# Kernel optimization log

Measured on AMD Instinct MI355X. Metric: run time of the kernel, lower is better.

## Reference

```python
import jax, jax.numpy as jnp
import numpy as np

B = 64
RX, RZ, RX_, RZ_ = 32, 16, 16, 8
TN = 1
STRIDE = 2
IN_DIM, OUT_DIM = 256, 512
KEY_DIM, H, ATTN_RATIO = 32, 8, 2
D = ATTN_RATIO * KEY_DIM            # per-head value dim = 64
DH = D * H                          # 512
NH_KD = KEY_DIM * H                 # 256
N = RX * RX + TN * RZ * RZ          # 1280 tokens (search + template)
N_ = RX_ * RX_ + TN * RZ_ * RZ_     # 320 subsampled query tokens
SCALE = KEY_DIM ** -0.5
EPS = 1e-5


def linear_bn(x, W, gamma, beta):
    # Linear (no bias) followed by BatchNorm1d in training mode over (B*N, C)
    y = jnp.einsum('bnc,oc->bno', x, W)
    m = y.mean(axis=(0, 1))
    v = y.var(axis=(0, 1))  # biased variance, as torch BN uses for normalization
    return (y - m) * jax.lax.rsqrt(v + EPS) * gamma + beta


def subsample(x):
    # stride-subsample the search-region tokens and each template's tokens
    b, n, c = x.shape
    parts = [x[:, :RX * RX].reshape(b, RX, RX, c)[:, ::STRIDE, ::STRIDE].reshape(b, -1, c)]
    for i in range(TN):
        s = RX * RX + i * RZ * RZ
        z = x[:, s:s + RZ * RZ].reshape(b, RZ, RZ, c)[:, ::STRIDE, ::STRIDE].reshape(b, -1, c)
        parts.append(z)
    return jnp.concatenate(parts, axis=1)


def setup_inputs() -> dict:
    key = jax.random.key(0)
    ks = jax.random.split(key, 4)
    return {
        'x': jax.random.normal(ks[0], (B, N, IN_DIM), dtype=jnp.float32),
        'W_kv': jax.random.normal(ks[1], (NH_KD + DH, IN_DIM), dtype=jnp.float32) * 0.02,
        'g_kv': jnp.ones((NH_KD + DH,), jnp.float32),
        'b_kv': jnp.zeros((NH_KD + DH,), jnp.float32),
        'W_q': jax.random.normal(ks[2], (NH_KD, IN_DIM), dtype=jnp.float32) * 0.02,
        'g_q': jnp.ones((NH_KD,), jnp.float32),
        'b_q': jnp.zeros((NH_KD,), jnp.float32),
        'W_p': jax.random.normal(ks[3], (OUT_DIM, DH), dtype=jnp.float32) * 0.02,
        'g_p': jnp.ones((OUT_DIM,), jnp.float32),
        'b_p': jnp.zeros((OUT_DIM,), jnp.float32),
    }


def reference(x, W_kv, g_kv, b_kv, W_q, g_q, b_q, W_p, g_p, b_p):
    b = x.shape[0]
    # fused KV projection + BN, then split into per-head K and V
    kv = linear_bn(x, W_kv, g_kv, b_kv).reshape(b, N, H, KEY_DIM + D)
    k = kv[..., :KEY_DIM].transpose(0, 2, 1, 3)   # [B,H,N,key_dim]
    v = kv[..., KEY_DIM:].transpose(0, 2, 1, 3)   # [B,H,N,d]
    # Q: subsample tokens, then Linear_BN
    q = linear_bn(subsample(x), W_q, g_q, b_q).reshape(b, N_, H, KEY_DIM).transpose(0, 2, 1, 3)
    attn = jax.nn.softmax(jnp.einsum('bhqd,bhkd->bhqk', q, k) * SCALE, axis=-1)
    o = jnp.einsum('bhqk,bhkd->bhqd', attn, v).transpose(0, 2, 1, 3).reshape(b, N_, DH)
    return linear_bn(jax.nn.hard_swish(o), W_p, g_p, b_p)
```

## Files before the change

### kernel.cpp

```cpp
#include <hip/hip_runtime.h>
#include <hip/hip_bf16.h>
#include <math.h>

#define EPSF 1e-5f
#define SCALEF 0.17677669529663687f
#define LOG2E 1.4426950408889634f

typedef unsigned short u16;
typedef unsigned int u32;
typedef __attribute__((ext_vector_type(8))) short bf16x8;
typedef __attribute__((ext_vector_type(4))) float f32x4;

__device__ __forceinline__ float b2f(u16 u) {
    union { unsigned int i; float f; } v; v.i = ((unsigned int)u) << 16; return v.f;
}
__device__ __forceinline__ u16 f2b(float f) {
    union { float f; unsigned int i; } v; v.f = f;
    unsigned int x = v.i;
    return (u16)((x + 0x7fffu + ((x >> 16) & 1u)) >> 16);
}
__device__ __forceinline__ float fexp2(float x) {
#if __has_builtin(__builtin_amdgcn_exp2f)
    return __builtin_amdgcn_exp2f(x);
#else
    return exp2f(x);
#endif
}
__device__ __forceinline__ u32 cvtpk_bf16(float lo, float hi) {
    u32 r;
    asm("v_cvt_pk_bf16_f32 %0, %1, %2" : "=v"(r) : "v"(lo), "v"(hi));
    return r;
}
__device__ __forceinline__ void gload_lds16(const u16* __restrict__ g, u16* l) {
    __builtin_amdgcn_global_load_lds(
        (const __attribute__((address_space(1))) void*)g,
        (__attribute__((address_space(3))) void*)l, 16, 0, 0);
}

__global__ void convert_f32_bf16(const float* __restrict__ src, u16* __restrict__ dst, int n4) {
    int i = blockIdx.x * 256 + threadIdx.x;
    if (i >= n4) return;
    float4 v = ((const float4*)src)[i];
    ushort4 o;
    o.x = f2b(v.x); o.y = f2b(v.y); o.z = f2b(v.z); o.w = f2b(v.w);
    ((ushort4*)dst)[i] = o;
}

__global__ void convert_wkv_perm(const float* __restrict__ W, u16* __restrict__ out) {
    int r = blockIdx.x, cl = threadIdx.x;
    int src = (r < 256) ? ((r >> 5) * 96 + (r & 31))
                        : (((r - 256) >> 6) * 96 + 32 + ((r - 256) & 63));
    out[r * 256 + cl] = f2b(W[src * 256 + cl]);
}

__global__ void gather_sub_bf16(const u16* __restrict__ xb, u16* __restrict__ xsub, int n8) {
    int i = blockIdx.x * 256 + threadIdx.x;
    if (i >= n8) return;
    int e = i << 3;
    int row = e >> 8;
    int col = e & 255;
    int b = row / 320;
    int t = row - b * 320;
    int n;
    if (t < 256) n = ((t >> 4) << 6) + ((t & 15) << 1);
    else { int tt = t - 256; n = 1024 + ((tt >> 3) << 5) + ((tt & 7) << 1); }
    *(int4*)(xsub + e) = *(const int4*)(xb + ((size_t)(b * 1280 + n)) * 256 + col);
}

template<int MODE>
__global__ __launch_bounds__(256) void gemm_bt(const u16* __restrict__ A, const u16* __restrict__ Bw,
                                               void* __restrict__ Cv, void* __restrict__ C2v,
                                               int M, int N, int K,
                                               float* __restrict__ sums) {
    __shared__ u16 As[2][128 * 32];
    __shared__ u16 Bs[2][128 * 32];
    __shared__ float sumbuf[4][64][2];
    const int tid = threadIdx.x;
    const int wave = tid >> 6, lane = tid & 63;
    const int quad = lane >> 4, lc = lane & 15;
    const int wr = wave >> 1, wc = wave & 1;
    const int m0 = blockIdx.y * 128, n0 = blockIdx.x * 128;

    const int srow = (wave << 5) + (lane >> 2);
    const int scol = (lane & 3) << 3;
    const int ldsoff = (wave << 5) * 32;
    const u16* gA0 = A  + (size_t)(m0 + srow) * K + scol;
    const u16* gA1 = A  + (size_t)(m0 + srow + 16) * K + scol;
    const u16* gB0 = Bw + (size_t)(n0 + srow) * K + scol;
    const u16* gB1 = Bw + (size_t)(n0 + srow + 16) * K + scol;

    f32x4 acc[4][4];
#pragma unroll
    for (int i = 0; i < 4; ++i)
#pragma unroll
        for (int j = 0; j < 4; ++j) acc[i][j] = (f32x4){0.f, 0.f, 0.f, 0.f};

    auto STAGE = [&](int buf, int k0) {
        gload_lds16(gA0 + k0, &As[buf][ldsoff]);
        gload_lds16(gA1 + k0, &As[buf][ldsoff + 16 * 32]);
        gload_lds16(gB0 + k0, &Bs[buf][ldsoff]);
        gload_lds16(gB1 + k0, &Bs[buf][ldsoff + 16 * 32]);
    };

    STAGE(0, 0);
    int cur = 0;
    for (int k0 = 0; k0 < K; k0 += 32) {
        if (k0 + 32 < K) {
            STAGE(cur ^ 1, k0 + 32);
            asm volatile("s_waitcnt vmcnt(4)" ::: "memory");
        } else {
            asm volatile("s_waitcnt vmcnt(0)" ::: "memory");
        }
        __builtin_amdgcn_s_barrier();
        bf16x8 af[4], bfr[4];
#pragma unroll
        for (int mi = 0; mi < 4; ++mi) af[mi]  = *(const bf16x8*)&As[cur][(wr * 64 + mi * 16 + lc) * 32 + quad * 8];
#pragma unroll
        for (int ni = 0; ni < 4; ++ni) bfr[ni] = *(const bf16x8*)&Bs[cur][(wc * 64 + ni * 16 + lc) * 32 + quad * 8];
#pragma unroll
        for (int mi = 0; mi < 4; ++mi)
#pragma unroll
            for (int ni = 0; ni < 4; ++ni)
                acc[mi][ni] = __builtin_amdgcn_mfma_f32_16x16x32_bf16(af[mi], bfr[ni], acc[mi][ni], 0, 0, 0);
        __builtin_amdgcn_s_barrier();
        cur ^= 1;
    }

    float ps[4], ps2[4];
#pragma unroll
    for (int ni = 0; ni < 4; ++ni) { ps[ni] = 0.f; ps2[ni] = 0.f; }
#pragma unroll
    for (int mi = 0; mi < 4; ++mi)
#pragma unroll
        for (int ni = 0; ni < 4; ++ni)
#pragma unroll
            for (int r = 0; r < 4; ++r) {
                float v = acc[mi][ni][r];
                ps[ni] += v; ps2[ni] += v * v;
            }

    if (MODE == 0 || MODE == 1) {
#pragma unroll
        for (int mi = 0; mi < 4; ++mi)
#pragma unroll
            for (int ni = 0; ni < 4; ++ni)
#pragma unroll
                for (int r = 0; r < 4; ++r) {
                    int row = m0 + wr * 64 + mi * 16 + quad * 4 + r;
                    int cn  = n0 + wc * 64 + ni * 16 + lc;
                    float v = acc[mi][ni][r];
                    if (MODE == 1) ((float*)Cv)[(size_t)row * N + cn] = v;
                    else           ((u16*)Cv)[(size_t)row * N + cn] = f2b(v);
                }
    } else if (n0 < 256) {
        u16* Kr = (u16*)Cv;
#pragma unroll
        for (int mi = 0; mi < 4; ++mi)
#pragma unroll
            for (int r = 0; r < 4; ++r) {
                int t = m0 + wr * 64 + mi * 16 + quad * 4 + r;
                int kk = t & 31;
                int pr = (t & ~31) + ((kk & 4) << 2) + ((kk >> 3) << 2) + (kk & 3);
#pragma unroll
                for (int ni = 0; ni < 4; ++ni) {
                    int c = n0 + wc * 64 + ni * 16 + lc;
                    Kr[(size_t)pr * 256 + c] = f2b(acc[mi][ni][r]);
                }
            }
    } else {
        u16* Vt = (u16*)C2v;
#pragma unroll
        for (int mi = 0; mi < 4; ++mi)
#pragma unroll
            for (int ni = 0; ni < 4; ++ni) {
                int cp = n0 - 256 + wc * 64 + ni * 16 + lc;
                int t0 = m0 + wr * 64 + mi * 16 + quad * 4;
                uint2 w;
                w.x = cvtpk_bf16(acc[mi][ni][0], acc[mi][ni][1]);
                w.y = cvtpk_bf16(acc[mi][ni][2], acc[mi][ni][3]);
                *(uint2*)(Vt + (size_t)cp * 81920 + t0) = w;
            }
    }

#pragma unroll
    for (int ni = 0; ni < 4; ++ni) {
        ps[ni]  += __shfl_xor(ps[ni], 16);  ps[ni]  += __shfl_xor(ps[ni], 32);
        ps2[ni] += __shfl_xor(ps2[ni], 16); ps2[ni] += __shfl_xor(ps2[ni], 32);
    }
    if (quad == 0) {
#pragma unroll
        for (int ni = 0; ni < 4; ++ni) {
            sumbuf[wave][ni * 16 + lc][0] = ps[ni];
            sumbuf[wave][ni * 16 + lc][1] = ps2[ni];
        }
    }
    __syncthreads();
    {
        int which = tid & 1, idx = (tid >> 1) & 63, wcg = tid >> 7;
        int channel = n0 + wcg * 64 + idx;
        float v = sumbuf[wcg][idx][which] + sumbuf[wcg + 2][idx][which];
        int rep = blockIdx.y & 7;
        atomicAdd(&sums[(rep * 2 + which) * N + channel], v);
    }
}

__global__ void finalize_bn(const float* __restrict__ sum2, const float* __restrict__ g,
                            const float* __restrict__ beta, int cols, float inv_n, float scale,
                            float* __restrict__ AB, int kvperm) {
    int c = blockIdx.x * 256 + threadIdx.x;
    if (c >= cols) return;
    float s = 0.f, s2 = 0.f;
#pragma unroll
    for (int r = 0; r < 8; ++r) {
        s  += sum2[(r * 2 + 0) * cols + c];
        s2 += sum2[(r * 2 + 1) * cols + c];
    }
    int src = c;
    if (kvperm) {
        src = (c < 256) ? ((c >> 5) * 96 + (c & 31))
                        : (((c - 256) >> 6) * 96 + 32 + ((c - 256) & 63));
    }
    float m = s * inv_n;
    float var = s2 * inv_n - m * m;
    float a = g[src] * rsqrtf(var + EPSF) * scale;
    AB[c] = a;
    AB[cols + c] = beta[src] * scale - m * a;
}

__global__ __launch_bounds__(256, 2) void attn_kernel5(const u16* __restrict__ Kr, const u16* __restrict__ Vt,
                                                       const u16* __restrict__ q_raw,
                                                       const float* __restrict__ ABq,
                                                       const float* __restrict__ ABkv,
                                                       u16* __restrict__ o_act) {
    const int tid = threadIdx.x;
    const int wave = tid >> 6, lane = tid & 63;
    const int quad = lane >> 4, lc = lane & 15;
    const int h = blockIdx.x, b = blockIdx.y;

    float qa[8], qb[8];
#pragma unroll
    for (int j = 0; j < 8; ++j) {
        int c = h * 32 + quad * 8 + j;
        float ak = ABkv[c];
        qa[j] = ABq[c] * ak;
        qb[j] = ABq[256 + c] * ak;
    }
    bf16x8 qf[5];
#pragma unroll
    for (int j = 0; j < 5; ++j) {
        const u16* qs = q_raw + ((size_t)(b * 320 + j * 64 + wave * 16 + lc)) * 256 + h * 32 + quad * 8;
        union { int4 v; u16 u[8]; } ld; ld.v = *(const int4*)qs;
        union { bf16x8 v; u16 u[8]; } st;
#pragma unroll
        for (int jj = 0; jj < 8; ++jj) st.u[jj] = f2b(b2f(ld.u[jj]) * qa[jj] + qb[jj]);
        qf[j] = st.v;
    }

    const u16* Kp = Kr + (size_t)b * 1280 * 256 + (size_t)lc * 256 + h * 32 + quad * 8;
    const u16* Vp = Vt + ((size_t)(h * 64 + lc)) * 81920 + b * 1280 + quad * 8;

    f32x4 acc[5][4];
#pragma unroll
    for (int j = 0; j < 5; ++j)
#pragma unroll
        for (int i = 0; i < 4; ++i) acc[j][i] = (f32x4){0.f, 0.f, 0.f, 0.f};
    float lsum[5];
#pragma unroll
    for (int j = 0; j < 5; ++j) lsum[j] = 0.f;

    const f32x4 z = (f32x4){0.f, 0.f, 0.f, 0.f};
    for (int kc = 0; kc < 1280; kc += 32) {
        bf16x8 kfA = *(const bf16x8*)(Kp + (size_t)kc * 256);
        bf16x8 kfB = *(const bf16x8*)(Kp + (size_t)(kc + 16) * 256);
        bf16x8 vf0 = *(const bf16x8*)(Vp + kc);
        bf16x8 vf1 = *(const bf16x8*)(Vp + (size_t)16 * 81920 + kc);
        bf16x8 vf2 = *(const bf16x8*)(Vp + (size_t)32 * 81920 + kc);
        bf16x8 vf3 = *(const bf16x8*)(Vp + (size_t)48 * 81920 + kc);
        f32x4 s0[5], s1[5];
#pragma unroll
        for (int j = 0; j < 5; ++j) {
            s0[j] = __builtin_amdgcn_mfma_f32_16x16x32_bf16(kfA, qf[j], z, 0, 0, 0);
            s1[j] = __builtin_amdgcn_mfma_f32_16x16x32_bf16(kfB, qf[j], z, 0, 0, 0);
        }
#pragma unroll
        for (int j = 0; j < 5; ++j) {
            float p0 = fexp2(s0[j][0]);
            float p1 = fexp2(s0[j][1]);
            float p2 = fexp2(s0[j][2]);
            float p3 = fexp2(s0[j][3]);
            float p4 = fexp2(s1[j][0]);
            float p5 = fexp2(s1[j][1]);
            float p6 = fexp2(s1[j][2]);
            float p7 = fexp2(s1[j][3]);
            lsum[j] += ((p0 + p1) + (p2 + p3)) + ((p4 + p5) + (p6 + p7));
            union { u32 w[4]; bf16x8 v; } pf;
            pf.w[0] = cvtpk_bf16(p0, p1);
            pf.w[1] = cvtpk_bf16(p2, p3);
            pf.w[2] = cvtpk_bf16(p4, p5);
            pf.w[3] = cvtpk_bf16(p6, p7);
            acc[j][0] = __builtin_amdgcn_mfma_f32_16x16x32_bf16(vf0, pf.v, acc[j][0], 0, 0, 0);
            acc[j][1] = __builtin_amdgcn_mfma_f32_16x16x32_bf16(vf1, pf.v, acc[j][1], 0, 0, 0);
            acc[j][2] = __builtin_amdgcn_mfma_f32_16x16x32_bf16(vf2, pf.v, acc[j][2], 0, 0, 0);
            acc[j][3] = __builtin_amdgcn_mfma_f32_16x16x32_bf16(vf3, pf.v, acc[j][3], 0, 0, 0);
        }
    }
    float av[16], bv[16];
#pragma unroll
    for (int t = 0; t < 16; ++t) {
        int cv = 256 + h * 64 + (t >> 2) * 16 + quad * 4 + (t & 3);
        av[t] = ABkv[cv];
        bv[t] = ABkv[768 + cv];
    }
#pragma unroll
    for (int j = 0; j < 5; ++j) {
        float l = lsum[j];
        l += __shfl_xor(l, 16);
        l += __shfl_xor(l, 32);
        float inv = 1.f / l;
        int qrow = b * 320 + j * 64 + wave * 16 + lc;
        u16* dst = o_act + (size_t)qrow * 512 + h * 64 + quad * 4;
#pragma unroll
        for (int nt = 0; nt < 4; ++nt) {
            ushort4 st;
#pragma unroll
            for (int r = 0; r < 4; ++r) {
                float o = av[nt * 4 + r] * (acc[j][nt][r] * inv) + bv[nt * 4 + r];
                float hs = o * fminf(fmaxf(o + 3.f, 0.f), 6.f) * (1.f / 6.f);
                ((u16*)&st)[r] = f2b(hs);
            }
            *(ushort4*)(dst + nt * 16) = st;
        }
    }
}

__global__ void bn_apply_out(const float* __restrict__ praw, const float* __restrict__ ABp,
                             float* __restrict__ out, int n4) {
    int i = blockIdx.x * 256 + threadIdx.x;
    if (i >= n4) return;
    int e = i << 2;
    int c = e & 511;
    float4 v = ((const float4*)praw)[i];
    float4 o;
    o.x = v.x * ABp[c]     + ABp[512 + c];
    o.y = v.y * ABp[c + 1] + ABp[512 + c + 1];
    o.z = v.z * ABp[c + 2] + ABp[512 + c + 2];
    o.w = v.w * ABp[c + 3] + ABp[512 + c + 3];
    ((float4*)out)[i] = o;
}

extern "C" void kernel_launch(void* const* d_in, const int* in_sizes, int n_in,
                              void* d_out, int out_size, void* d_ws, size_t ws_size,
                              hipStream_t stream) {
    const float* x   = (const float*)d_in[0];
    const float* Wkv = (const float*)d_in[1];
    const float* gkv = (const float*)d_in[2];
    const float* bkv = (const float*)d_in[3];
    const float* Wq  = (const float*)d_in[4];
    const float* gq  = (const float*)d_in[5];
    const float* bq  = (const float*)d_in[6];
    const float* Wp  = (const float*)d_in[7];
    const float* gp  = (const float*)d_in[8];
    const float* bp  = (const float*)d_in[9];
    float* out = (float*)d_out;

    char* ws = (char*)d_ws;
    size_t off = 0;
    auto alloc = [&](size_t bytes) -> void* {
        void* p = ws + off;
        off += (bytes + 255) & ~(size_t)255;
        return p;
    };
    void*  slot1  = alloc(81920ull * 256 * 2);
    u16*   x_b    = (u16*)slot1;
    float* p_raw  = (float*)slot1;
    u16*   K_raw  = (u16*)alloc(81920ull * 256 * 2);
    u16*   Vt_raw = (u16*)alloc(512ull * 81920 * 2);
    u16*   q_raw  = (u16*)alloc(20480ull * 256 * 2);
    void*  slot2  = alloc(20480ull * 512 * 2);
    u16*   xsub_b = (u16*)slot2;
    u16*   o_act  = (u16*)slot2;
    u16*   Wkv_b  = (u16*)alloc(768ull * 256 * 2);
    u16*   Wq_b   = (u16*)alloc(256ull * 256 * 2);
    u16*   Wp_b   = (u16*)alloc(512ull * 512 * 2);
    float* sums_kv = (float*)alloc(8 * 2 * 768 * sizeof(float));
    float* sums_q  = (float*)alloc(8 * 2 * 256 * sizeof(float));
    float* sums_p  = (float*)alloc(8 * 2 * 512 * sizeof(float));
    float* ABkv = (float*)alloc(1536 * sizeof(float));
    float* ABq  = (float*)alloc(512 * sizeof(float));
    float* ABp  = (float*)alloc(1024 * sizeof(float));

    dim3 blk(256);
    hipMemsetAsync(sums_kv, 0, 8 * 2 * (768 + 256 + 512) * sizeof(float), stream);

    convert_f32_bf16<<<20480, blk, 0, stream>>>(x,   x_b,   5242880);
    convert_wkv_perm<<<768,   blk, 0, stream>>>(Wkv, Wkv_b);
    convert_f32_bf16<<<64,    blk, 0, stream>>>(Wq,  Wq_b,  16384);
    convert_f32_bf16<<<256,   blk, 0, stream>>>(Wp,  Wp_b,  65536);
    gather_sub_bf16<<<2560,   blk, 0, stream>>>(x_b, xsub_b, 655360);

    gemm_bt<2><<<dim3(6, 640), blk, 0, stream>>>(x_b, Wkv_b, K_raw, Vt_raw, 81920, 768, 256, sums_kv);
    gemm_bt<0><<<dim3(2, 160), blk, 0, stream>>>(xsub_b, Wq_b, q_raw, nullptr, 20480, 256, 256, sums_q);

    finalize_bn<<<3, blk, 0, stream>>>(sums_kv, gkv, bkv, 768, 1.f / 81920.f, 1.f, ABkv, 1);
    finalize_bn<<<1, blk, 0, stream>>>(sums_q,  gq,  bq,  256, 1.f / 20480.f, SCALEF * LOG2E, ABq, 0);

    attn_kernel5<<<dim3(8, 64), blk, 0, stream>>>(K_raw, Vt_raw, q_raw, ABq, ABkv, o_act);

    gemm_bt<1><<<dim3(4, 160), blk, 0, stream>>>(o_act, Wp_b, p_raw, nullptr, 20480, 512, 512, sums_p);
    finalize_bn<<<2, blk, 0, stream>>>(sums_p, gp, bp, 512, 1.f / 20480.f, 1.f, ABp, 0);

    bn_apply_out<<<10240, blk, 0, stream>>>(p_raw, ABp, out, 2621440);
}
```

Before: 353.4 us.

## Replace LDS-staged GEMM with single-wave direct-load GEMM and XCD-aware tile mapping

```diff
diff --git a/kernel.cpp b/kernel.cpp
--- a/kernel.cpp
+++ b/kernel.cpp
@@ -30,11 +30,6 @@
     u32 r;
     asm("v_cvt_pk_bf16_f32 %0, %1, %2" : "=v"(r) : "v"(lo), "v"(hi));
     return r;
-}
-__device__ __forceinline__ void gload_lds16(const u16* __restrict__ g, u16* l) {
-    __builtin_amdgcn_global_load_lds(
-        (const __attribute__((address_space(1))) void*)g,
-        (__attribute__((address_space(3))) void*)l, 16, 0, 0);
 }
 
 __global__ void convert_f32_bf16(const float* __restrict__ src, u16* __restrict__ dst, int n4) {
@@ -67,27 +62,22 @@
     *(int4*)(xsub + e) = *(const int4*)(xb + ((size_t)(b * 1280 + n)) * 256 + col);
 }
 
-template<int MODE>
-__global__ __launch_bounds__(256) void gemm_bt(const u16* __restrict__ A, const u16* __restrict__ Bw,
-                                               void* __restrict__ Cv, void* __restrict__ C2v,
-                                               int M, int N, int K,
-                                               float* __restrict__ sums) {
-    __shared__ u16 As[2][128 * 32];
-    __shared__ u16 Bs[2][128 * 32];
-    __shared__ float sumbuf[4][64][2];
-    const int tid = threadIdx.x;
-    const int wave = tid >> 6, lane = tid & 63;
+template<int MODE, int NT, int KC>
+__global__ __launch_bounds__(64) void gemm1w(const u16* __restrict__ A, const u16* __restrict__ Bw,
+                                             void* __restrict__ Cv, void* __restrict__ C2v,
+                                             int N, float* __restrict__ sums) {
+    const int lane = threadIdx.x;
     const int quad = lane >> 4, lc = lane & 15;
-    const int wr = wave >> 1, wc = wave & 1;
-    const int m0 = blockIdx.y * 128, n0 = blockIdx.x * 128;
-
-    const int srow = (wave << 5) + (lane >> 2);
-    const int scol = (lane & 3) << 3;
-    const int ldsoff = (wave << 5) * 32;
-    const u16* gA0 = A  + (size_t)(m0 + srow) * K + scol;
-    const u16* gA1 = A  + (size_t)(m0 + srow + 16) * K + scol;
-    const u16* gB0 = Bw + (size_t)(n0 + srow) * K + scol;
-    const u16* gB1 = Bw + (size_t)(n0 + srow + 16) * K + scol;
+    const int id = blockIdx.x;
+    const int xcd = id & 7;
+    const int l = id >> 3;
+    const int mchunk = (int)(gridDim.x >> 3) / NT;
+    const int m_t = xcd * mchunk + l / NT;
+    const int n_t = l % NT;
+    const int m0 = m_t * 64, n0 = n_t * 64;
+
+    const u16* Ap = A  + (size_t)(m0 + lc) * KC + quad * 8;
+    const u16* Bp = Bw + (size_t)(n0 + lc) * KC + quad * 8;
 
     f32x4 acc[4][4];
 #pragma unroll
@@ -95,35 +85,18 @@
 #pragma unroll
         for (int j = 0; j < 4; ++j) acc[i][j] = (f32x4){0.f, 0.f, 0.f, 0.f};
 
-    auto STAGE = [&](int buf, int k0) {
-        gload_lds16(gA0 + k0, &As[buf][ldsoff]);
-        gload_lds16(gA1 + k0, &As[buf][ldsoff + 16 * 32]);
-        gload_lds16(gB0 + k0, &Bs[buf][ldsoff]);
-        gload_lds16(gB1 + k0, &Bs[buf][ldsoff + 16 * 32]);
-    };
-
-    STAGE(0, 0);
-    int cur = 0;
-    for (int k0 = 0; k0 < K; k0 += 32) {
-        if (k0 + 32 < K) {
-            STAGE(cur ^ 1, k0 + 32);
-            asm volatile("s_waitcnt vmcnt(4)" ::: "memory");
-        } else {
-            asm volatile("s_waitcnt vmcnt(0)" ::: "memory");
-        }
-        __builtin_amdgcn_s_barrier();
+#pragma unroll 2
+    for (int k0 = 0; k0 < KC; k0 += 32) {
         bf16x8 af[4], bfr[4];
 #pragma unroll
-        for (int mi = 0; mi < 4; ++mi) af[mi]  = *(const bf16x8*)&As[cur][(wr * 64 + mi * 16 + lc) * 32 + quad * 8];
-#pragma unroll
-        for (int ni = 0; ni < 4; ++ni) bfr[ni] = *(const bf16x8*)&Bs[cur][(wc * 64 + ni * 16 + lc) * 32 + quad * 8];
+        for (int mi = 0; mi < 4; ++mi) af[mi]  = *(const bf16x8*)(Ap + (size_t)(mi * 16) * KC + k0);
+#pragma unroll
+        for (int ni = 0; ni < 4; ++ni) bfr[ni] = *(const bf16x8*)(Bp + (size_t)(ni * 16) * KC + k0);
 #pragma unroll
         for (int mi = 0; mi < 4; ++mi)
 #pragma unroll
             for (int ni = 0; ni < 4; ++ni)
                 acc[mi][ni] = __builtin_amdgcn_mfma_f32_16x16x32_bf16(af[mi], bfr[ni], acc[mi][ni], 0, 0, 0);
-        __builtin_amdgcn_s_barrier();
-        cur ^= 1;
     }
 
     float ps[4], ps2[4];
@@ -138,6 +111,20 @@
                 float v = acc[mi][ni][r];
                 ps[ni] += v; ps2[ni] += v * v;
             }
+#pragma unroll
+    for (int ni = 0; ni < 4; ++ni) {
+        ps[ni]  += __shfl_xor(ps[ni], 16);  ps[ni]  += __shfl_xor(ps[ni], 32);
+        ps2[ni] += __shfl_xor(ps2[ni], 16); ps2[ni] += __shfl_xor(ps2[ni], 32);
+    }
+    if (quad == 0) {
+        int rep = m_t & 7;
+#pragma unroll
+        for (int ni = 0; ni < 4; ++ni) {
+            int c = n0 + ni * 16 + lc;
+            atomicAdd(&sums[(rep * 2 + 0) * N + c], ps[ni]);
+            atomicAdd(&sums[(rep * 2 + 1) * N + c], ps2[ni]);
+        }
+    }
 
     if (MODE == 0 || MODE == 1) {
 #pragma unroll
@@ -146,8 +133,8 @@
             for (int ni = 0; ni < 4; ++ni)
 #pragma unroll
                 for (int r = 0; r < 4; ++r) {
-                    int row = m0 + wr * 64 + mi * 16 + quad * 4 + r;
-                    int cn  = n0 + wc * 64 + ni * 16 + lc;
+                    int row = m0 + mi * 16 + quad * 4 + r;
+                    int cn  = n0 + ni * 16 + lc;
                     float v = acc[mi][ni][r];
                     if (MODE == 1) ((float*)Cv)[(size_t)row * N + cn] = v;
                     else           ((u16*)Cv)[(size_t)row * N + cn] = f2b(v);
@@ -158,12 +145,12 @@
         for (int mi = 0; mi < 4; ++mi)
 #pragma unroll
             for (int r = 0; r < 4; ++r) {
-                int t = m0 + wr * 64 + mi * 16 + quad * 4 + r;
+                int t = m0 + mi * 16 + quad * 4 + r;
                 int kk = t & 31;
                 int pr = (t & ~31) + ((kk & 4) << 2) + ((kk >> 3) << 2) + (kk & 3);
 #pragma unroll
                 for (int ni = 0; ni < 4; ++ni) {
-                    int c = n0 + wc * 64 + ni * 16 + lc;
+                    int c = n0 + ni * 16 + lc;
                     Kr[(size_t)pr * 256 + c] = f2b(acc[mi][ni][r]);
                 }
             }
@@ -173,34 +160,13 @@
         for (int mi = 0; mi < 4; ++mi)
 #pragma unroll
             for (int ni = 0; ni < 4; ++ni) {
-                int cp = n0 - 256 + wc * 64 + ni * 16 + lc;
-                int t0 = m0 + wr * 64 + mi * 16 + quad * 4;
+                int cp = n0 - 256 + ni * 16 + lc;
+                int t0 = m0 + mi * 16 + quad * 4;
                 uint2 w;
                 w.x = cvtpk_bf16(acc[mi][ni][0], acc[mi][ni][1]);
                 w.y = cvtpk_bf16(acc[mi][ni][2], acc[mi][ni][3]);
                 *(uint2*)(Vt + (size_t)cp * 81920 + t0) = w;
             }
-    }
-
-#pragma unroll
-    for (int ni = 0; ni < 4; ++ni) {
-        ps[ni]  += __shfl_xor(ps[ni], 16);  ps[ni]  += __shfl_xor(ps[ni], 32);
-        ps2[ni] += __shfl_xor(ps2[ni], 16); ps2[ni] += __shfl_xor(ps2[ni], 32);
-    }
-    if (quad == 0) {
-#pragma unroll
-        for (int ni = 0; ni < 4; ++ni) {
-            sumbuf[wave][ni * 16 + lc][0] = ps[ni];
-            sumbuf[wave][ni * 16 + lc][1] = ps2[ni];
-        }
-    }
-    __syncthreads();
-    {
-        int which = tid & 1, idx = (tid >> 1) & 63, wcg = tid >> 7;
-        int channel = n0 + wcg * 64 + idx;
-        float v = sumbuf[wcg][idx][which] + sumbuf[wcg + 2][idx][which];
-        int rep = blockIdx.y & 7;
-        atomicAdd(&sums[(rep * 2 + which) * N + channel], v);
     }
 }
 
@@ -398,15 +364,15 @@
     convert_f32_bf16<<<256,   blk, 0, stream>>>(Wp,  Wp_b,  65536);
     gather_sub_bf16<<<2560,   blk, 0, stream>>>(x_b, xsub_b, 655360);
 
-    gemm_bt<2><<<dim3(6, 640), blk, 0, stream>>>(x_b, Wkv_b, K_raw, Vt_raw, 81920, 768, 256, sums_kv);
-    gemm_bt<0><<<dim3(2, 160), blk, 0, stream>>>(xsub_b, Wq_b, q_raw, nullptr, 20480, 256, 256, sums_q);
+    gemm1w<2, 12, 256><<<15360, 64, 0, stream>>>(x_b,    Wkv_b, K_raw, Vt_raw, 768, sums_kv);
+    gemm1w<0, 4,  256><<<1280,  64, 0, stream>>>(xsub_b, Wq_b,  q_raw, nullptr, 256, sums_q);
 
     finalize_bn<<<3, blk, 0, stream>>>(sums_kv, gkv, bkv, 768, 1.f / 81920.f, 1.f, ABkv, 1);
     finalize_bn<<<1, blk, 0, stream>>>(sums_q,  gq,  bq,  256, 1.f / 20480.f, SCALEF * LOG2E, ABq, 0);
 
     attn_kernel5<<<dim3(8, 64), blk, 0, stream>>>(K_raw, Vt_raw, q_raw, ABq, ABkv, o_act);
 
-    gemm_bt<1><<<dim3(4, 160), blk, 0, stream>>>(o_act, Wp_b, p_raw, nullptr, 20480, 512, 512, sums_p);
+    gemm1w<1, 8, 512><<<2560, 64, 0, stream>>>(o_act, Wp_b, p_raw, nullptr, 512, sums_p);
     finalize_bn<<<2, blk, 0, stream>>>(sums_p, gp, bp, 512, 1.f / 20480.f, 1.f, ABp, 0);
 
     bn_apply_out<<<10240, blk, 0, stream>>>(p_raw, ABp, out, 2621440);
```

Result: slower. 431.1 us (+22.0%).

## Single-buffer GEMM LDS and remap blocks to XCD-contiguous M chunks

Applied to the files above, without the earlier changes.

```diff
diff --git a/kernel.cpp b/kernel.cpp
--- a/kernel.cpp
+++ b/kernel.cpp
@@ -67,23 +67,30 @@
     *(int4*)(xsub + e) = *(const int4*)(xb + ((size_t)(b * 1280 + n)) * 256 + col);
 }
 
-template<int MODE>
+template<int MODE, int NT>
 __global__ __launch_bounds__(256) void gemm_bt(const u16* __restrict__ A, const u16* __restrict__ Bw,
                                                void* __restrict__ Cv, void* __restrict__ C2v,
-                                               int M, int N, int K,
-                                               float* __restrict__ sums) {
-    __shared__ u16 As[2][128 * 32];
-    __shared__ u16 Bs[2][128 * 32];
+                                               int N, int K, float* __restrict__ sums) {
+    __shared__ u16 As[128 * 32];
+    __shared__ u16 Bs[128 * 32];
     __shared__ float sumbuf[4][64][2];
     const int tid = threadIdx.x;
     const int wave = tid >> 6, lane = tid & 63;
     const int quad = lane >> 4, lc = lane & 15;
     const int wr = wave >> 1, wc = wave & 1;
-    const int m0 = blockIdx.y * 128, n0 = blockIdx.x * 128;
+    const int id = blockIdx.x;
+    const int xcd = id & 7, l = id >> 3;
+    const int mchunk = ((int)gridDim.x >> 3) / NT;
+    const int m_t = xcd * mchunk + l / NT;
+    const int n_t = l - (l / NT) * NT;
+    const int m0 = m_t * 128, n0 = n_t * 128;
 
     const int srow = (wave << 5) + (lane >> 2);
     const int scol = (lane & 3) << 3;
-    const int ldsoff = (wave << 5) * 32;
+    u16* ldsA0 = As + ((wave << 5) + 0) * 32;
+    u16* ldsA1 = As + ((wave << 5) + 16) * 32;
+    u16* ldsB0 = Bs + ((wave << 5) + 0) * 32;
+    u16* ldsB1 = Bs + ((wave << 5) + 16) * 32;
     const u16* gA0 = A  + (size_t)(m0 + srow) * K + scol;
     const u16* gA1 = A  + (size_t)(m0 + srow + 16) * K + scol;
     const u16* gB0 = Bw + (size_t)(n0 + srow) * K + scol;
@@ -95,35 +102,24 @@
 #pragma unroll
         for (int j = 0; j < 4; ++j) acc[i][j] = (f32x4){0.f, 0.f, 0.f, 0.f};
 
-    auto STAGE = [&](int buf, int k0) {
-        gload_lds16(gA0 + k0, &As[buf][ldsoff]);
-        gload_lds16(gA1 + k0, &As[buf][ldsoff + 16 * 32]);
-        gload_lds16(gB0 + k0, &Bs[buf][ldsoff]);
-        gload_lds16(gB1 + k0, &Bs[buf][ldsoff + 16 * 32]);
-    };
-
-    STAGE(0, 0);
-    int cur = 0;
     for (int k0 = 0; k0 < K; k0 += 32) {
-        if (k0 + 32 < K) {
-            STAGE(cur ^ 1, k0 + 32);
-            asm volatile("s_waitcnt vmcnt(4)" ::: "memory");
-        } else {
-            asm volatile("s_waitcnt vmcnt(0)" ::: "memory");
-        }
-        __builtin_amdgcn_s_barrier();
+        __syncthreads();
+        gload_lds16(gA0 + k0, ldsA0);
+        gload_lds16(gA1 + k0, ldsA1);
+        gload_lds16(gB0 + k0, ldsB0);
+        gload_lds16(gB1 + k0, ldsB1);
+        asm volatile("s_waitcnt vmcnt(0)" ::: "memory");
+        __syncthreads();
         bf16x8 af[4], bfr[4];
 #pragma unroll
-        for (int mi = 0; mi < 4; ++mi) af[mi]  = *(const bf16x8*)&As[cur][(wr * 64 + mi * 16 + lc) * 32 + quad * 8];
-#pragma unroll
-        for (int ni = 0; ni < 4; ++ni) bfr[ni] = *(const bf16x8*)&Bs[cur][(wc * 64 + ni * 16 + lc) * 32 + quad * 8];
+        for (int mi = 0; mi < 4; ++mi) af[mi]  = *(const bf16x8*)&As[(wr * 64 + mi * 16 + lc) * 32 + quad * 8];
+#pragma unroll
+        for (int ni = 0; ni < 4; ++ni) bfr[ni] = *(const bf16x8*)&Bs[(wc * 64 + ni * 16 + lc) * 32 + quad * 8];
 #pragma unroll
         for (int mi = 0; mi < 4; ++mi)
 #pragma unroll
             for (int ni = 0; ni < 4; ++ni)
                 acc[mi][ni] = __builtin_amdgcn_mfma_f32_16x16x32_bf16(af[mi], bfr[ni], acc[mi][ni], 0, 0, 0);
-        __builtin_amdgcn_s_barrier();
-        cur ^= 1;
     }
 
     float ps[4], ps2[4];
@@ -199,7 +195,7 @@
         int which = tid & 1, idx = (tid >> 1) & 63, wcg = tid >> 7;
         int channel = n0 + wcg * 64 + idx;
         float v = sumbuf[wcg][idx][which] + sumbuf[wcg + 2][idx][which];
-        int rep = blockIdx.y & 7;
+        int rep = m_t & 7;
         atomicAdd(&sums[(rep * 2 + which) * N + channel], v);
     }
 }
@@ -398,15 +394,15 @@
     convert_f32_bf16<<<256,   blk, 0, stream>>>(Wp,  Wp_b,  65536);
     gather_sub_bf16<<<2560,   blk, 0, stream>>>(x_b, xsub_b, 655360);
 
-    gemm_bt<2><<<dim3(6, 640), blk, 0, stream>>>(x_b, Wkv_b, K_raw, Vt_raw, 81920, 768, 256, sums_kv);
-    gemm_bt<0><<<dim3(2, 160), blk, 0, stream>>>(xsub_b, Wq_b, q_raw, nullptr, 20480, 256, 256, sums_q);
+    gemm_bt<2, 6><<<3840, blk, 0, stream>>>(x_b,    Wkv_b, K_raw, Vt_raw, 768, 256, sums_kv);
+    gemm_bt<0, 2><<<320,  blk, 0, stream>>>(xsub_b, Wq_b,  q_raw, nullptr, 256, 256, sums_q);
 
     finalize_bn<<<3, blk, 0, stream>>>(sums_kv, gkv, bkv, 768, 1.f / 81920.f, 1.f, ABkv, 1);
     finalize_bn<<<1, blk, 0, stream>>>(sums_q,  gq,  bq,  256, 1.f / 20480.f, SCALEF * LOG2E, ABq, 0);
 
     attn_kernel5<<<dim3(8, 64), blk, 0, stream>>>(K_raw, Vt_raw, q_raw, ABq, ABkv, o_act);
 
-    gemm_bt<1><<<dim3(4, 160), blk, 0, stream>>>(o_act, Wp_b, p_raw, nullptr, 20480, 512, 512, sums_p);
+    gemm_bt<1, 4><<<640, blk, 0, stream>>>(o_act, Wp_b, p_raw, nullptr, 512, 512, sums_p);
     finalize_bn<<<2, blk, 0, stream>>>(sums_p, gp, bp, 512, 1.f / 20480.f, 1.f, ABp, 0);
 
     bn_apply_out<<<10240, blk, 0, stream>>>(p_raw, ABp, out, 2621440);
```

New measurement: 351.0 us. No clear change (-0.7%).
